# Kernel optimization log

Measured on AMD Instinct MI355X. Metric: run time of the kernel, lower is better.

Reference implementation:

```python
import jax, jax.numpy as jnp
import numpy as np

N_LAYERS = 3

def setup_inputs() -> dict:
    key = jax.random.key(0)
    ks = jax.random.split(key, 16)
    N, E, F_in, H = 50000, 800000, 5, 64
    x = jax.random.normal(ks[0], (N, F_in), dtype=jnp.float32)
    edge_index = jax.random.randint(ks[1], (2, E), 0, N, dtype=jnp.int64)
    s = lambda fan_in: 1.0 / np.sqrt(fan_in)
    return {
        "x": x,
        "edge_index": edge_index,
        "W_enc": jax.random.uniform(ks[2], (F_in, H), jnp.float32, -s(F_in), s(F_in)),
        "b_enc": jnp.zeros((H,), jnp.float32),
        "conv_W": jax.random.uniform(ks[3], (N_LAYERS, H, H), jnp.float32, -s(H), s(H)),
        "conv_b": jnp.zeros((N_LAYERS, H), jnp.float32),
        "W_d1": jax.random.uniform(ks[4], (H, H // 2), jnp.float32, -s(H), s(H)),
        "b_d1": jnp.zeros((H // 2,), jnp.float32),
        "W_d2": jax.random.uniform(ks[5], (H // 2, 1), jnp.float32, -s(H // 2), s(H // 2)),
        "b_d2": jnp.zeros((1,), jnp.float32),
        "W_i1": jax.random.uniform(ks[6], (H, H // 2), jnp.float32, -s(H), s(H)),
        "b_i1": jnp.zeros((H // 2,), jnp.float32),
        "W_i2": jax.random.uniform(ks[7], (H // 2, 1), jnp.float32, -s(H // 2), s(H // 2)),
        "b_i2": jnp.zeros((1,), jnp.float32),
    }

def reference(x, edge_index, W_enc, b_enc, conv_W, conv_b,
              W_d1, b_d1, W_d2, b_d2, W_i1, b_i1, W_i2, b_i2):
    N = x.shape[0]
    # GCN normalization with self-loops (PyG GCNConv default):
    loops = jnp.arange(N, dtype=edge_index.dtype)
    row = jnp.concatenate([edge_index[0], loops])  # source
    col = jnp.concatenate([edge_index[1], loops])  # target
    deg = jax.ops.segment_sum(jnp.ones_like(row, dtype=x.dtype), col, num_segments=N)
    dinv = jax.lax.rsqrt(deg)  # deg >= 1 due to self-loops
    norm = dinv[row] * dinv[col]  # [E + N]

    h = jax.nn.relu(x @ W_enc + b_enc)  # [N, H]
    for l in range(N_LAYERS):
        hw = h @ conv_W[l]                       # [N, H]
        msg = hw[row] * norm[:, None]            # gather + scale
        agg = jax.ops.segment_sum(msg, col, num_segments=N)  # scatter-add
        h = jax.nn.relu(agg + conv_b[l])

    demand = jax.nn.relu(h @ W_d1 + b_d1) @ W_d2 + b_d2       # [N, 1]
    inventory = jax.nn.relu(h @ W_i1 + b_i1) @ W_i2 + b_i2    # [N, 1]
    return (demand, inventory)
```

## Files before the change

### kernel.cpp

```cpp
#include <hip/hip_runtime.h>
#include <hip/hip_bf16.h>


#define HDIM 64
#define PB 256
#define NPB 256
#define NPB_SHIFT 8
#define BCAP 8192

__device__ inline unsigned bfpack(float lo, float hi) {
    unsigned ul = __float_as_uint(lo), uh = __float_as_uint(hi);
    ul += 0x7fffu + ((ul >> 16) & 1u);
    uh += 0x7fffu + ((uh >> 16) & 1u);
    return (ul >> 16) | (uh & 0xffff0000u);
}

__device__ inline float2 bfunpack(unsigned u) {
    float2 r;
    r.x = __uint_as_float(u << 16);
    r.y = __uint_as_float(u & 0xffff0000u);
    return r;
}

__global__ __launch_bounds__(256) void hist_pass(const int* __restrict__ dst,
                                                 unsigned* __restrict__ histT,
                                                 int E, int NB) {
    __shared__ unsigned h[256];
    int t = threadIdx.x, p = blockIdx.x;
    h[t] = 0u;
    __syncthreads();
    int chunk = (E + PB - 1) / PB;
    int lo = p * chunk, hi = min(lo + chunk, E);
    for (int e = lo + t; e < hi; e += 256)
        atomicAdd(&h[dst[e] >> NPB_SHIFT], 1u);
    __syncthreads();
    if (t < NB) histT[t * PB + p] = h[t];
}

__global__ __launch_bounds__(PB) void scan_bucket(unsigned* __restrict__ histT,
                                                  unsigned* __restrict__ btot) {
    __shared__ unsigned s[PB];
    int t = threadIdx.x, k = blockIdx.x;
    unsigned v = histT[k * PB + t];
    s[t] = v;
    __syncthreads();
#pragma unroll
    for (int off = 1; off < PB; off <<= 1) {
        unsigned u = (t >= off) ? s[t - off] : 0u;
        __syncthreads();
        s[t] += u;
        __syncthreads();
    }
    histT[k * PB + t] = s[t] - v;
    if (t == PB - 1) btot[k] = s[t];
}

__global__ __launch_bounds__(256) void bin_pass(const int* __restrict__ ei,
                                                const unsigned* __restrict__ histT,
                                                const unsigned* __restrict__ btot,
                                                unsigned* __restrict__ ebuf,
                                                int E, int NB) {
    __shared__ unsigned bb[256];
    __shared__ unsigned cur[256];
    int t = threadIdx.x, p = blockIdx.x;
    unsigned bv = (t < NB) ? btot[t] : 0u;
    bb[t] = bv;
    __syncthreads();
#pragma unroll
    for (int off = 1; off < 256; off <<= 1) {
        unsigned u = (t >= off) ? bb[t - off] : 0u;
        __syncthreads();
        bb[t] += u;
        __syncthreads();
    }
    if (t < NB) cur[t] = histT[t * PB + p] + (bb[t] - bv);
    __syncthreads();
    int chunk = (E + PB - 1) / PB;
    int lo = p * chunk, hi = min(lo + chunk, E);
    for (int e = lo + t; e < hi; e += 256) {
        unsigned sN = (unsigned)ei[e];
        unsigned dN = (unsigned)ei[E + e];
        unsigned pos = atomicAdd(&cur[dN >> NPB_SHIFT], 1u);
        ebuf[pos] = ((dN & (NPB - 1u)) << 16) | sN;
    }
}

__global__ __launch_bounds__(256) void csr_pass(const unsigned* __restrict__ ebuf,
                                                const unsigned* __restrict__ btot,
                                                unsigned* __restrict__ row_ptr,
                                                unsigned short* __restrict__ pc8,
                                                float* __restrict__ dinv,
                                                int* __restrict__ csr_pad,
                                                int N, int E, int NB) {
    __shared__ unsigned bb[256];
    __shared__ unsigned cntL[NPB];
    __shared__ unsigned sc[NPB];
    __shared__ unsigned cur[NPB];
    int t = threadIdx.x, k = blockIdx.x;
    unsigned bv = (t < NB) ? btot[t] : 0u;
    bb[t] = bv;
    __syncthreads();
#pragma unroll
    for (int off = 1; off < 256; off <<= 1) {
        unsigned u = (t >= off) ? bb[t - off] : 0u;
        __syncthreads();
        bb[t] += u;
        __syncthreads();
    }
    unsigned e1 = bb[k];
    unsigned e0 = e1 - btot[k];
    int nbase = k << NPB_SHIFT;
    cntL[t] = 0u;
    __syncthreads();
    for (unsigned e = e0 + t; e < e1; e += 256)
        atomicAdd(&cntL[ebuf[e] >> 16], 1u);
    __syncthreads();
    unsigned v = cntL[t];
    unsigned pcnt = (v + 7u) & ~7u;
    sc[t] = pcnt;
    __syncthreads();
#pragma unroll
    for (int off = 1; off < NPB; off <<= 1) {
        unsigned u = (t >= off) ? sc[t - off] : 0u;
        __syncthreads();
        sc[t] += u;
        __syncthreads();
    }
    unsigned pos0 = (unsigned)k * BCAP + (sc[t] - pcnt);
    cur[t] = pos0;
    int node = nbase + t;
    if (node < N) {
        row_ptr[node] = pos0;
        pc8[node] = (unsigned short)(pcnt >> 3);
        dinv[node] = rsqrtf((float)(v + 1u));
        for (unsigned j = v; j < pcnt; j++) csr_pad[pos0 + j] = N;
    }
    __syncthreads();
    for (unsigned e = e0 + t; e < e1; e += 256) {
        unsigned ed = ebuf[e];
        unsigned pos = atomicAdd(&cur[ed >> 16], 1u);
        csr_pad[pos] = (int)(ed & 0xffffu);
    }
}

__global__ __launch_bounds__(256) void encoder(const float* __restrict__ x,
                                               const float* __restrict__ W,
                                               const float* __restrict__ b,
                                               const float* __restrict__ dinv,
                                               unsigned* __restrict__ hnA,
                                               unsigned* __restrict__ hnB, int N) {
    int t = blockIdx.x * 256 + threadIdx.x;
    int i = t >> 5, jp = t & 31;
    if (i > N) return;
    if (i == N) {
        hnA[t] = 0u;
        hnB[t] = 0u;
        return;
    }
    int j0 = 2 * jp;
    float a0 = b[j0], a1 = b[j0 + 1];
#pragma unroll
    for (int k = 0; k < 5; k++) {
        float xv = x[i * 5 + k];
        a0 = fmaf(xv, W[k * 64 + j0], a0);
        a1 = fmaf(xv, W[k * 64 + j0 + 1], a1);
    }
    float di = dinv[i];
    hnA[t] = bfpack(di * fmaxf(a0, 0.0f), di * fmaxf(a1, 0.0f));
}

#define ACC4(A, V) do {                                                         \
    float2 _p = bfunpack((V).x), _q = bfunpack((V).y);                          \
    (A).x += _p.x; (A).y += _p.y; (A).z += _q.x; (A).w += _q.y;                 \
} while (0)

__device__ inline float4 gather_pad_q(const int* __restrict__ idx, int nb,
                                      const uint2* __restrict__ hp, int fl,
                                      float4 a0) {
    float4 a1 = {0.f, 0.f, 0.f, 0.f}, a2 = a1, a3 = a1;
    if (nb > 0) {
        int s0 = idx[0], s1 = idx[1], s2 = idx[2], s3 = idx[3];
        int s4 = idx[4], s5 = idx[5], s6 = idx[6], s7 = idx[7];
        int u = 0;
        while (true) {
            uint2 v0 = hp[(size_t)s0 * 16 + fl];
            uint2 v1 = hp[(size_t)s1 * 16 + fl];
            uint2 v2 = hp[(size_t)s2 * 16 + fl];
            uint2 v3 = hp[(size_t)s3 * 16 + fl];
            uint2 v4 = hp[(size_t)s4 * 16 + fl];
            uint2 v5 = hp[(size_t)s5 * 16 + fl];
            uint2 v6 = hp[(size_t)s6 * 16 + fl];
            uint2 v7 = hp[(size_t)s7 * 16 + fl];
            u += 8;
            bool more = (u >> 3) < nb;
            if (more) {
                s0 = idx[u + 0]; s1 = idx[u + 1]; s2 = idx[u + 2]; s3 = idx[u + 3];
                s4 = idx[u + 4]; s5 = idx[u + 5]; s6 = idx[u + 6]; s7 = idx[u + 7];
            }
            ACC4(a0, v0); ACC4(a1, v1); ACC4(a2, v2); ACC4(a3, v3);
            ACC4(a0, v4); ACC4(a1, v5); ACC4(a2, v6); ACC4(a3, v7);
            if (!more) break;
        }
    }
    a0.x += a1.x; a0.y += a1.y; a0.z += a1.z; a0.w += a1.w;
    a2.x += a3.x; a2.y += a3.y; a2.z += a3.z; a2.w += a3.w;
    a0.x += a2.x; a0.y += a2.y; a0.z += a2.z; a0.w += a2.w;
    return a0;
}

#define CONV_K8(WROW, HK) do {                                                  \
    float4 wa = ((const float4*)(WROW))[0];                                     \
    float4 wb = ((const float4*)(WROW))[1];                                     \
    acc0.x = fmaf(HK, wa.x, acc0.x); acc0.y = fmaf(HK, wa.y, acc0.y);           \
    acc0.z = fmaf(HK, wa.z, acc0.z); acc0.w = fmaf(HK, wa.w, acc0.w);           \
    acc1.x = fmaf(HK, wb.x, acc1.x); acc1.y = fmaf(HK, wb.y, acc1.y);           \
    acc1.z = fmaf(HK, wb.z, acc1.z); acc1.w = fmaf(HK, wb.w, acc1.w);           \
} while (0)

__global__ __launch_bounds__(512, 4) void gconv(const unsigned* __restrict__ row_ptr,
                                                const unsigned short* __restrict__ pc8,
                                                const int* __restrict__ csr_pad,
                                                const unsigned* __restrict__ hn_in,
                                                const float* __restrict__ W,
                                                const float* __restrict__ b,
                                                const float* __restrict__ dinv,
                                                unsigned* __restrict__ hn_out, int N) {
    __shared__ float ybuf[64 * 65];
    int tid = threadIdx.x;
    int qw = tid >> 4, fl = tid & 15;
    int base = blockIdx.x * 64;
    const uint2* hp = (const uint2*)hn_in;
    for (int s = 0; s < 2; s++) {
        int n = qw * 2 + s;
        int i = base + n;
        if (i < N) {
            uint2 sv = hp[(size_t)i * 16 + fl];
            float4 a;
            float2 p = bfunpack(sv.x), q = bfunpack(sv.y);
            a.x = p.x; a.y = p.y; a.z = q.x; a.w = q.y;
            a = gather_pad_q(csr_pad + row_ptr[i], (int)pc8[i], hp, fl, a);
            ybuf[(4 * fl + 0) * 65 + n] = a.x;
            ybuf[(4 * fl + 1) * 65 + n] = a.y;
            ybuf[(4 * fl + 2) * 65 + n] = a.z;
            ybuf[(4 * fl + 3) * 65 + n] = a.w;
        }
    }
    __syncthreads();
    int n = tid & 63;
    int qt = __builtin_amdgcn_readfirstlane(tid >> 6);
    int i = base + n;
    if (i >= N) return;
    int jb = qt * 8;
    float di = dinv[i];
    float4 acc0 = {0.f, 0.f, 0.f, 0.f}, acc1 = acc0;
    const float* Wj = W + jb;
#pragma unroll
    for (int k = 0; k < 64; k++) {
        float hk = ybuf[k * 65 + n];
        CONV_K8(Wj + k * 64, hk);
    }
    const float* bj = b + jb;
    float4 y0, y1;
    y0.x = fmaxf(fmaf(di, acc0.x, bj[0]), 0.f) * di;
    y0.y = fmaxf(fmaf(di, acc0.y, bj[1]), 0.f) * di;
    y0.z = fmaxf(fmaf(di, acc0.z, bj[2]), 0.f) * di;
    y0.w = fmaxf(fmaf(di, acc0.w, bj[3]), 0.f) * di;
    y1.x = fmaxf(fmaf(di, acc1.x, bj[4]), 0.f) * di;
    y1.y = fmaxf(fmaf(di, acc1.y, bj[5]), 0.f) * di;
    y1.z = fmaxf(fmaf(di, acc1.z, bj[6]), 0.f) * di;
    y1.w = fmaxf(fmaf(di, acc1.w, bj[7]), 0.f) * di;
    uint4 p;
    p.x = bfpack(y0.x, y0.y);
    p.y = bfpack(y0.z, y0.w);
    p.z = bfpack(y1.x, y1.y);
    p.w = bfpack(y1.z, y1.w);
    *(uint4*)(hn_out + (size_t)i * 32 + qt * 4) = p;
}

__global__ __launch_bounds__(512, 4) void gconv_heads(const unsigned* __restrict__ row_ptr,
                                                      const unsigned short* __restrict__ pc8,
                                                      const int* __restrict__ csr_pad,
                                                      const unsigned* __restrict__ hn_in,
                                                      const float* __restrict__ W,
                                                      const float* __restrict__ b,
                                                      const float* __restrict__ dinv,
                                                      const float* __restrict__ W_d1, const float* __restrict__ b_d1,
                                                      const float* __restrict__ W_d2, const float* __restrict__ b_d2,
                                                      const float* __restrict__ W_i1, const float* __restrict__ b_i1,
                                                      const float* __restrict__ W_i2, const float* __restrict__ b_i2,
                                                      float* __restrict__ out, int N) {
    __shared__ float ybuf[64 * 65];
    __shared__ float opart[512];
    int tid = threadIdx.x;
    int qw = tid >> 4, fl = tid & 15;
    int base = blockIdx.x * 64;
    const uint2* hp = (const uint2*)hn_in;
    for (int s = 0; s < 2; s++) {
        int n = qw * 2 + s;
        int i = base + n;
        if (i < N) {
            uint2 sv = hp[(size_t)i * 16 + fl];
            float4 a;
            float2 p = bfunpack(sv.x), q = bfunpack(sv.y);
            a.x = p.x; a.y = p.y; a.z = q.x; a.w = q.y;
            a = gather_pad_q(csr_pad + row_ptr[i], (int)pc8[i], hp, fl, a);
            ybuf[(4 * fl + 0) * 65 + n] = a.x;
            ybuf[(4 * fl + 1) * 65 + n] = a.y;
            ybuf[(4 * fl + 2) * 65 + n] = a.z;
            ybuf[(4 * fl + 3) * 65 + n] = a.w;
        }
    }
    __syncthreads();
    int n = tid & 63;
    int qt = __builtin_amdgcn_readfirstlane(tid >> 6);
    int i = base + n;
    int jb = qt * 8;
    float y[8];
    if (i < N) {
        float di = dinv[i];
        float4 acc0 = {0.f, 0.f, 0.f, 0.f}, acc1 = acc0;
        const float* Wj = W + jb;
#pragma unroll
        for (int k = 0; k < 64; k++) {
            float hk = ybuf[k * 65 + n];
            CONV_K8(Wj + k * 64, hk);
        }
        const float* bj = b + jb;
        y[0] = fmaxf(fmaf(di, acc0.x, bj[0]), 0.f);
        y[1] = fmaxf(fmaf(di, acc0.y, bj[1]), 0.f);
        y[2] = fmaxf(fmaf(di, acc0.z, bj[2]), 0.f);
        y[3] = fmaxf(fmaf(di, acc0.w, bj[3]), 0.f);
        y[4] = fmaxf(fmaf(di, acc1.x, bj[4]), 0.f);
        y[5] = fmaxf(fmaf(di, acc1.y, bj[5]), 0.f);
        y[6] = fmaxf(fmaf(di, acc1.z, bj[6]), 0.f);
        y[7] = fmaxf(fmaf(di, acc1.w, bj[7]), 0.f);
    }
    __syncthreads();
    if (i < N) {
#pragma unroll
        for (int jj = 0; jj < 8; jj++) ybuf[(jb + jj) * 65 + n] = y[jj];
    }
    __syncthreads();
    int hd = __builtin_amdgcn_readfirstlane(tid >> 8);
    int q2 = __builtin_amdgcn_readfirstlane((tid >> 6) & 3);
    int hb = q2 * 8;
    float op = 0.f;
    if (i < N) {
        const float* W1 = (hd ? W_i1 : W_d1) + hb;
        const float* b1 = (hd ? b_i1 : b_d1) + hb;
        const float* W2 = (hd ? W_i2 : W_d2) + hb;
        float4 acc0 = {0.f, 0.f, 0.f, 0.f}, acc1 = acc0;
#pragma unroll
        for (int k = 0; k < 64; k++) {
            float hk = ybuf[k * 65 + n];
            CONV_K8(W1 + k * 32, hk);
        }
        op = fmaf(fmaxf(acc0.x + b1[0], 0.f), W2[0], op);
        op = fmaf(fmaxf(acc0.y + b1[1], 0.f), W2[1], op);
        op = fmaf(fmaxf(acc0.z + b1[2], 0.f), W2[2], op);
        op = fmaf(fmaxf(acc0.w + b1[3], 0.f), W2[3], op);
        op = fmaf(fmaxf(acc1.x + b1[4], 0.f), W2[4], op);
        op = fmaf(fmaxf(acc1.y + b1[5], 0.f), W2[5], op);
        op = fmaf(fmaxf(acc1.z + b1[6], 0.f), W2[6], op);
        op = fmaf(fmaxf(acc1.w + b1[7], 0.f), W2[7], op);
    }
    opart[tid] = op;
    __syncthreads();
    if (tid < 128) {
        int n2 = tid & 63, h2 = tid >> 6;
        int i2 = base + n2;
        if (i2 < N) {
            int o0 = h2 * 256 + n2;
            float o = opart[o0] + opart[o0 + 64] + opart[o0 + 128] + opart[o0 + 192]
                    + (h2 ? b_i2[0] : b_d2[0]);
            out[(size_t)h2 * N + i2] = o;
        }
    }
}

extern "C" void kernel_launch(void* const* d_in, const int* in_sizes, int n_in,
                              void* d_out, int out_size, void* d_ws, size_t ws_size,
                              hipStream_t stream) {
    const float* x      = (const float*)d_in[0];
    const int*   ei     = (const int*)d_in[1];
    const float* W_enc  = (const float*)d_in[2];
    const float* b_enc  = (const float*)d_in[3];
    const float* conv_W = (const float*)d_in[4];
    const float* conv_b = (const float*)d_in[5];
    const float* W_d1   = (const float*)d_in[6];
    const float* b_d1   = (const float*)d_in[7];
    const float* W_d2   = (const float*)d_in[8];
    const float* b_d2   = (const float*)d_in[9];
    const float* W_i1   = (const float*)d_in[10];
    const float* b_i1   = (const float*)d_in[11];
    const float* W_i2   = (const float*)d_in[12];
    const float* b_i2   = (const float*)d_in[13];

    const int N = in_sizes[0] / 5;
    const int E = in_sizes[1] / 2;
    const int NB = (N + NPB - 1) >> NPB_SHIFT;

    unsigned* hnA = (unsigned*)d_ws;
    unsigned* hnB = hnA + (size_t)(N + 1) * 32;
    float* dinv = (float*)(hnB + (size_t)(N + 1) * 32);
    unsigned* row_ptr = (unsigned*)(dinv + N);
    unsigned short* pc8 = (unsigned short*)(row_ptr + N);
    unsigned* histT = (unsigned*)(pc8 + N);
    unsigned* btot  = histT + (size_t)NB * PB;
    int* csr_pad    = (int*)(btot + NB);
    unsigned* ebuf  = (unsigned*)d_ws;
    float* out = (float*)d_out;

    const int gBlocks = (N + 63) / 64;

    hist_pass<<<PB, 256, 0, stream>>>(ei + E, histT, E, NB);
    scan_bucket<<<NB, PB, 0, stream>>>(histT, btot);
    bin_pass<<<PB, 256, 0, stream>>>(ei, histT, btot, ebuf, E, NB);
    csr_pass<<<NB, 256, 0, stream>>>(ebuf, btot, row_ptr, pc8, dinv, csr_pad, N, E, NB);

    encoder<<<((N + 1) * 32 + 255) / 256, 256, 0, stream>>>(x, W_enc, b_enc, dinv,
                                                            hnA, hnB, N);

    gconv<<<gBlocks, 512, 0, stream>>>(row_ptr, pc8, csr_pad, hnA,
                                       conv_W + 0 * HDIM * HDIM, conv_b + 0 * HDIM,
                                       dinv, hnB, N);
    gconv<<<gBlocks, 512, 0, stream>>>(row_ptr, pc8, csr_pad, hnB,
                                       conv_W + 1 * HDIM * HDIM, conv_b + 1 * HDIM,
                                       dinv, hnA, N);
    gconv_heads<<<gBlocks, 512, 0, stream>>>(row_ptr, pc8, csr_pad, hnA,
                                             conv_W + 2 * HDIM * HDIM, conv_b + 2 * HDIM,
                                             dinv, W_d1, b_d1, W_d2, b_d2,
                                             W_i1, b_i1, W_i2, b_i2, out, N);
}
```

Baseline: 207.2 us.

## Build CSR with global-atomic degree count and direct scatter instead of bucket sort

```diff
diff --git a/kernel.cpp b/kernel.cpp
--- a/kernel.cpp
+++ b/kernel.cpp
@@ -3,7 +3,6 @@
 
 
 #define HDIM 64
-#define PB 256
 #define NPB 256
 #define NPB_SHIFT 8
 #define BCAP 8192
@@ -22,100 +21,29 @@
     return r;
 }
 
-__global__ __launch_bounds__(256) void hist_pass(const int* __restrict__ dst,
-                                                 unsigned* __restrict__ histT,
-                                                 int E, int NB) {
-    __shared__ unsigned h[256];
-    int t = threadIdx.x, p = blockIdx.x;
-    h[t] = 0u;
-    __syncthreads();
-    int chunk = (E + PB - 1) / PB;
-    int lo = p * chunk, hi = min(lo + chunk, E);
-    for (int e = lo + t; e < hi; e += 256)
-        atomicAdd(&h[dst[e] >> NPB_SHIFT], 1u);
-    __syncthreads();
-    if (t < NB) histT[t * PB + p] = h[t];
-}
-
-__global__ __launch_bounds__(PB) void scan_bucket(unsigned* __restrict__ histT,
-                                                  unsigned* __restrict__ btot) {
-    __shared__ unsigned s[PB];
+__global__ __launch_bounds__(256) void zero_deg(unsigned* __restrict__ deg, int N) {
+    int i = blockIdx.x * 256 + threadIdx.x;
+    if (i < N) deg[i] = 0u;
+}
+
+__global__ __launch_bounds__(256) void deg_pass(const int* __restrict__ dst,
+                                                unsigned* __restrict__ deg, int E) {
+    int stride = gridDim.x * 256;
+    for (int e = blockIdx.x * 256 + threadIdx.x; e < E; e += stride)
+        atomicAdd(&deg[dst[e]], 1u);
+}
+
+__global__ __launch_bounds__(256) void scan_nodes(const unsigned* __restrict__ deg,
+                                                  unsigned* __restrict__ row_ptr,
+                                                  unsigned short* __restrict__ pc8,
+                                                  float* __restrict__ dinv,
+                                                  unsigned* __restrict__ cur,
+                                                  int* __restrict__ csr_pad,
+                                                  int N) {
+    __shared__ unsigned sc[NPB];
     int t = threadIdx.x, k = blockIdx.x;
-    unsigned v = histT[k * PB + t];
-    s[t] = v;
-    __syncthreads();
-#pragma unroll
-    for (int off = 1; off < PB; off <<= 1) {
-        unsigned u = (t >= off) ? s[t - off] : 0u;
-        __syncthreads();
-        s[t] += u;
-        __syncthreads();
-    }
-    histT[k * PB + t] = s[t] - v;
-    if (t == PB - 1) btot[k] = s[t];
-}
-
-__global__ __launch_bounds__(256) void bin_pass(const int* __restrict__ ei,
-                                                const unsigned* __restrict__ histT,
-                                                const unsigned* __restrict__ btot,
-                                                unsigned* __restrict__ ebuf,
-                                                int E, int NB) {
-    __shared__ unsigned bb[256];
-    __shared__ unsigned cur[256];
-    int t = threadIdx.x, p = blockIdx.x;
-    unsigned bv = (t < NB) ? btot[t] : 0u;
-    bb[t] = bv;
-    __syncthreads();
-#pragma unroll
-    for (int off = 1; off < 256; off <<= 1) {
-        unsigned u = (t >= off) ? bb[t - off] : 0u;
-        __syncthreads();
-        bb[t] += u;
-        __syncthreads();
-    }
-    if (t < NB) cur[t] = histT[t * PB + p] + (bb[t] - bv);
-    __syncthreads();
-    int chunk = (E + PB - 1) / PB;
-    int lo = p * chunk, hi = min(lo + chunk, E);
-    for (int e = lo + t; e < hi; e += 256) {
-        unsigned sN = (unsigned)ei[e];
-        unsigned dN = (unsigned)ei[E + e];
-        unsigned pos = atomicAdd(&cur[dN >> NPB_SHIFT], 1u);
-        ebuf[pos] = ((dN & (NPB - 1u)) << 16) | sN;
-    }
-}
-
-__global__ __launch_bounds__(256) void csr_pass(const unsigned* __restrict__ ebuf,
-                                                const unsigned* __restrict__ btot,
-                                                unsigned* __restrict__ row_ptr,
-                                                unsigned short* __restrict__ pc8,
-                                                float* __restrict__ dinv,
-                                                int* __restrict__ csr_pad,
-                                                int N, int E, int NB) {
-    __shared__ unsigned bb[256];
-    __shared__ unsigned cntL[NPB];
-    __shared__ unsigned sc[NPB];
-    __shared__ unsigned cur[NPB];
-    int t = threadIdx.x, k = blockIdx.x;
-    unsigned bv = (t < NB) ? btot[t] : 0u;
-    bb[t] = bv;
-    __syncthreads();
-#pragma unroll
-    for (int off = 1; off < 256; off <<= 1) {
-        unsigned u = (t >= off) ? bb[t - off] : 0u;
-        __syncthreads();
-        bb[t] += u;
-        __syncthreads();
-    }
-    unsigned e1 = bb[k];
-    unsigned e0 = e1 - btot[k];
-    int nbase = k << NPB_SHIFT;
-    cntL[t] = 0u;
-    __syncthreads();
-    for (unsigned e = e0 + t; e < e1; e += 256)
-        atomicAdd(&cntL[ebuf[e] >> 16], 1u);
-    __syncthreads();
-    unsigned v = cntL[t];
+    int node = (k << NPB_SHIFT) + t;
+    unsigned v = (node < N) ? deg[node] : 0u;
     unsigned pcnt = (v + 7u) & ~7u;
     sc[t] = pcnt;
     __syncthreads();
@@ -127,19 +55,25 @@
         __syncthreads();
     }
     unsigned pos0 = (unsigned)k * BCAP + (sc[t] - pcnt);
-    cur[t] = pos0;
-    int node = nbase + t;
     if (node < N) {
         row_ptr[node] = pos0;
         pc8[node] = (unsigned short)(pcnt >> 3);
         dinv[node] = rsqrtf((float)(v + 1u));
+        cur[node] = pos0;
         for (unsigned j = v; j < pcnt; j++) csr_pad[pos0 + j] = N;
     }
-    __syncthreads();
-    for (unsigned e = e0 + t; e < e1; e += 256) {
-        unsigned ed = ebuf[e];
-        unsigned pos = atomicAdd(&cur[ed >> 16], 1u);
-        csr_pad[pos] = (int)(ed & 0xffffu);
+}
+
+__global__ __launch_bounds__(256) void scatter_pass(const int* __restrict__ ei,
+                                                    unsigned* __restrict__ cur,
+                                                    int* __restrict__ csr_pad,
+                                                    int E) {
+    int stride = gridDim.x * 256;
+    for (int e = blockIdx.x * 256 + threadIdx.x; e < E; e += stride) {
+        int s = ei[e];
+        int d = ei[E + e];
+        unsigned pos = atomicAdd(&cur[d], 1u);
+        csr_pad[pos] = s;
     }
 }
 
@@ -405,18 +339,17 @@
     float* dinv = (float*)(hnB + (size_t)(N + 1) * 32);
     unsigned* row_ptr = (unsigned*)(dinv + N);
     unsigned short* pc8 = (unsigned short*)(row_ptr + N);
-    unsigned* histT = (unsigned*)(pc8 + N);
-    unsigned* btot  = histT + (size_t)NB * PB;
-    int* csr_pad    = (int*)(btot + NB);
-    unsigned* ebuf  = (unsigned*)d_ws;
+    unsigned* deg = (unsigned*)(pc8 + N);
+    unsigned* cur = deg + N;
+    int* csr_pad  = (int*)(cur + N);
     float* out = (float*)d_out;
 
     const int gBlocks = (N + 63) / 64;
 
-    hist_pass<<<PB, 256, 0, stream>>>(ei + E, histT, E, NB);
-    scan_bucket<<<NB, PB, 0, stream>>>(histT, btot);
-    bin_pass<<<PB, 256, 0, stream>>>(ei, histT, btot, ebuf, E, NB);
-    csr_pass<<<NB, 256, 0, stream>>>(ebuf, btot, row_ptr, pc8, dinv, csr_pad, N, E, NB);
+    zero_deg<<<(N + 255) / 256, 256, 0, stream>>>(deg, N);
+    deg_pass<<<2048, 256, 0, stream>>>(ei + E, deg, E);
+    scan_nodes<<<NB, 256, 0, stream>>>(deg, row_ptr, pc8, dinv, cur, csr_pad, N);
+    scatter_pass<<<2048, 256, 0, stream>>>(ei, cur, csr_pad, E);
 
     encoder<<<((N + 1) * 32 + 255) / 256, 256, 0, stream>>>(x, W_enc, b_enc, dinv,
                                                             hnA, hnB, N);
```

Result: slower. 265.1 us (+27.9%).
